# Optimization experiments

Measured on AMD Instinct MI355X. Metric: run time of the kernel, lower is better.

## Reference

```python
import jax, jax.numpy as jnp
import numpy as np

N_GRAPHS = 1250
NEG_SLOPE = 0.2

def gat_layer(x, src, dst, W, a_src, a_dst, b, concat):
    # x: [N, Fin]; W: [Fin, H*C]; a_src/a_dst: [H, C]; b: [H*C] or [C]
    N = x.shape[0]
    H, C = a_src.shape
    h = (x @ W).reshape(N, H, C)                      # [N,H,C]
    alpha_s = jnp.sum(h * a_src[None], axis=-1)       # [N,H]
    alpha_d = jnp.sum(h * a_dst[None], axis=-1)       # [N,H]
    e = jax.nn.leaky_relu(alpha_s[src] + alpha_d[dst], NEG_SLOPE)  # [E,H]
    # segment softmax over incoming edges of each target node
    m = jax.ops.segment_max(e, dst, num_segments=N)   # [N,H]
    m = jnp.where(jnp.isfinite(m), m, 0.0)
    ex = jnp.exp(e - m[dst])
    s = jax.ops.segment_sum(ex, dst, num_segments=N)  # [N,H]
    alpha = ex / (s[dst] + 1e-16)                     # [E,H]
    msg = h[src] * alpha[..., None]                   # [E,H,C]
    out = jax.ops.segment_sum(msg, dst, num_segments=N)  # [N,H,C]
    out = out.reshape(N, H * C) if concat else out.mean(axis=1)
    return out + b

def setup_inputs() -> dict:
    key = jax.random.key(0)
    ks = jax.random.split(key, 13)
    N, E = 50000, 100000
    x = jax.random.normal(ks[0], (N, 78), dtype=jnp.float32)
    edge_index = jax.random.randint(ks[1], (2, E), 0, N, dtype=jnp.int64)
    # sorted segment ids -> every graph non-empty (~40 nodes each)
    batch = jnp.sort(jax.random.randint(ks[2], (N,), 0, N_GRAPHS, dtype=jnp.int64))
    g = lambda k, shape, fan: jax.random.normal(k, shape, dtype=jnp.float32) / np.float32(np.sqrt(fan))
    return {
        'x': x, 'edge_index': edge_index, 'batch': batch,
        'W1': g(ks[3], (78, 780), 78), 'a_src1': g(ks[4], (10, 78), 78), 'a_dst1': g(ks[5], (10, 78), 78),
        'b1': jnp.zeros((780,), jnp.float32),
        'W2': g(ks[6], (780, 128), 780), 'a_src2': g(ks[7], (1, 128), 128), 'a_dst2': g(ks[8], (1, 128), 128),
        'b2': jnp.zeros((128,), jnp.float32),
        'fc_w': g(ks[9], (128, 128), 128), 'fc_b': jnp.zeros((128,), jnp.float32),
    }

def reference(x, edge_index, batch, W1, a_src1, a_dst1, b1, W2, a_src2, a_dst2, b2, fc_w, fc_b):
    N = x.shape[0]
    loop = jnp.arange(N, dtype=edge_index.dtype)
    src = jnp.concatenate([edge_index[0], loop])  # add self loops (PyG default)
    dst = jnp.concatenate([edge_index[1], loop])
    # dropout layers are identity in eval mode
    h = jax.nn.elu(gat_layer(x, src, dst, W1, a_src1, a_dst1, b1, concat=True))   # [N,780]
    h = jax.nn.relu(gat_layer(h, src, dst, W2, a_src2, a_dst2, b2, concat=True))  # [N,128]
    g = jax.ops.segment_max(h, batch, num_segments=N_GRAPHS)                      # [G,128]
    g = jnp.where(jnp.isfinite(g), g, 0.0)
    return jax.nn.relu(g @ fc_w + fc_b)
```

## Files before the change

kernel.cpp:

```cpp
#include <hip/hip_runtime.h>
#include <hip/hip_bf16.h>
#include <cstdint>

#define CAP 32
typedef __hip_bfloat16 bf16;
typedef __attribute__((ext_vector_type(8))) short short8;
typedef __attribute__((ext_vector_type(4))) float f32x4;

__device__ __forceinline__ float sb2f(short s) {
  unsigned int u = ((unsigned int)(unsigned short)s) << 16;
  return __uint_as_float(u);
}
__device__ __forceinline__ short f2sb(float f) {
  bf16 h = __float2bfloat16(f);
  return *reinterpret_cast<short*>(&h);
}

__global__ void k_detect(const int* __restrict__ ei, int* __restrict__ flag) {
  __shared__ int any;
  if (threadIdx.x == 0) any = 0;
  __syncthreads();
  int v = 0;
  for (int i = 1 + 2 * threadIdx.x; i < 2000; i += 512) v |= ei[i];
  if (v) atomicOr(&any, 1);
  __syncthreads();
  if (threadIdx.x == 0) flag[0] = (any == 0) ? 1 : 0;
}

__device__ __forceinline__ void edge_sd(const int* __restrict__ ei, int e, int f,
                                        int& src, int& dst) {
  if (e < 100000) {
    if (f) { src = ei[2 * e]; dst = ei[200000 + 2 * e]; }
    else   { src = ei[e];     dst = ei[100000 + e]; }
  } else { src = dst = e - 100000; }
  src = min(max(src, 0), 49999);
  dst = min(max(dst, 0), 49999);
}

__global__ void k_prep(const float* __restrict__ x, const float* __restrict__ W1,
                       const float* __restrict__ W2, const float* __restrict__ aw1,
                       const float* __restrict__ dw1, bf16* __restrict__ xb,
                       bf16* __restrict__ W1t, bf16* __restrict__ W2t,
                       bf16* __restrict__ Wat, float* __restrict__ zp, int zeroWords) {
  int i = blockIdx.x * 256 + threadIdx.x;
  if (i < zeroWords) zp[i] = 0.f;
  const int n_xb = 50000 * 96;
  const int n_w1 = 832 * 96;
  const int n_w2 = 128 * 832;
  const int n_wa = 32 * 96;
  if (i < n_xb) {
    int r = i / 96, k = i - r * 96;
    xb[i] = __float2bfloat16(k < 78 ? x[r * 78 + k] : 0.f);
  } else if (i < n_xb + n_w1) {
    int j = i - n_xb;
    int n = j / 96, k = j - n * 96;
    W1t[j] = __float2bfloat16((k < 78 && n < 780) ? W1[k * 780 + n] : 0.f);
  } else if (i < n_xb + n_w1 + n_w2) {
    int j = i - n_xb - n_w1;
    int c = j / 832, k = j - c * 832;
    W2t[j] = __float2bfloat16(k < 780 ? W2[k * 128 + c] : 0.f);
  } else if (i < n_xb + n_w1 + n_w2 + n_wa) {
    int j = i - n_xb - n_w1 - n_w2;
    int c = j / 96, k = j - c * 96;
    float s = 0.f;
    if (k < 78 && c < 20) {
      const float* w = (c < 10) ? aw1 : dw1;
      int h = (c < 10) ? c : c - 10;
      const float* wrow = W1 + k * 780 + h * 78;
      const float* arow = w + h * 78;
      for (int q = 0; q < 78; q++) s += wrow[q] * arow[q];
    }
    Wat[c * 96 + k] = __float2bfloat16(s);
  }
}

__global__ __launch_bounds__(256) void k_gemm1(const bf16* __restrict__ xb,
                                               const bf16* __restrict__ W1t,
                                               const bf16* __restrict__ Wat,
                                               bf16* __restrict__ H1,
                                               float* __restrict__ as1,
                                               float* __restrict__ ad1) {
  __shared__ __align__(16) short Als[64 * 104];
  __shared__ __align__(16) short Bls[64 * 104];
  __shared__ __align__(16) short Wls[32 * 104];
  __shared__ __align__(16) float Cls[64 * 68];
  const int t = threadIdx.x;
  const int w = t >> 6, l = t & 63, l15 = l & 15, q = l >> 4;
  const int rowBase = blockIdx.x * 64;
  for (int s = t; s < 768; s += 256) {
    int row = s / 12, kg = s - row * 12;
    short8 v = {};
    int gr = rowBase + row;
    if (gr < 50000) v = *(const short8*)((const short*)xb + (size_t)gr * 96 + kg * 8);
    *(short8*)&Als[row * 104 + kg * 8] = v;
  }
  for (int s = t; s < 384; s += 256) {
    int row = s / 12, kg = s - row * 12;
    *(short8*)&Wls[row * 104 + kg * 8] =
        *(const short8*)((const short*)Wat + (size_t)row * 96 + kg * 8);
  }
  short8 breg[3];
  int bn[3], bk[3];
#pragma unroll
  for (int i = 0; i < 3; i++) {
    int s = t + i * 256;
    bn[i] = s / 12; bk[i] = s - bn[i] * 12;
    breg[i] = *(const short8*)((const short*)W1t + (size_t)bn[i] * 96 + bk[i] * 8);
  }
  for (int cc = 0; cc < 13; cc++) {
    __syncthreads();
#pragma unroll
    for (int i = 0; i < 3; i++) *(short8*)&Bls[bn[i] * 104 + bk[i] * 8] = breg[i];
    if (cc < 12) {
#pragma unroll
      for (int i = 0; i < 3; i++)
        breg[i] = *(const short8*)((const short*)W1t +
                                   (size_t)((cc + 1) * 64 + bn[i]) * 96 + bk[i] * 8);
    }
    __syncthreads();
    f32x4 acc[4] = {};
#pragma unroll
    for (int ks = 0; ks < 3; ks++) {
      short8 a = *(const short8*)&Als[(w * 16 + l15) * 104 + ks * 32 + q * 8];
#pragma unroll
      for (int nt = 0; nt < 4; nt++) {
        short8 b = *(const short8*)&Bls[(nt * 16 + l15) * 104 + ks * 32 + q * 8];
        acc[nt] = __builtin_amdgcn_mfma_f32_16x16x32_bf16(a, b, acc[nt], 0, 0, 0);
      }
    }
    __syncthreads();
#pragma unroll
    for (int nt = 0; nt < 4; nt++)
#pragma unroll
      for (int r = 0; r < 4; r++)
        Cls[(w * 16 + q * 4 + r) * 68 + nt * 16 + l15] = acc[nt][r];
    __syncthreads();
    {
      int r = t >> 2, c0 = (t & 3) * 16;
      int gr = rowBase + r;
      if (gr < 50000) {
        short8 o0, o1;
#pragma unroll
        for (int c = 0; c < 8; c++) o0[c] = f2sb(Cls[r * 68 + c0 + c]);
#pragma unroll
        for (int c = 0; c < 8; c++) o1[c] = f2sb(Cls[r * 68 + c0 + 8 + c]);
        short* dst = (short*)H1 + (size_t)gr * 832 + cc * 64 + c0;
        *(short8*)dst = o0;
        *(short8*)(dst + 8) = o1;
      }
    }
  }
  f32x4 acc2[2] = {};
#pragma unroll
  for (int ks = 0; ks < 3; ks++) {
    short8 a = *(const short8*)&Als[(w * 16 + l15) * 104 + ks * 32 + q * 8];
#pragma unroll
    for (int nt = 0; nt < 2; nt++) {
      short8 b = *(const short8*)&Wls[(nt * 16 + l15) * 104 + ks * 32 + q * 8];
      acc2[nt] = __builtin_amdgcn_mfma_f32_16x16x32_bf16(a, b, acc2[nt], 0, 0, 0);
    }
  }
  const int gr0 = rowBase + w * 16 + q * 4;
#pragma unroll
  for (int nt = 0; nt < 2; nt++) {
    int c = nt * 16 + l15;
#pragma unroll
    for (int r = 0; r < 4; r++) {
      int gr = gr0 + r;
      if (gr < 50000) {
        if (c < 10)       as1[gr * 10 + c] = acc2[nt][r];
        else if (c < 20)  ad1[gr * 10 + (c - 10)] = acc2[nt][r];
      }
    }
  }
}

__global__ void k_scatter(const int* __restrict__ ei, const int* __restrict__ flag,
                          int* __restrict__ cnt, int* __restrict__ csr) {
  int e = blockIdx.x * 256 + threadIdx.x;
  if (e >= 150000) return;
  int f = flag[0], src, dst;
  edge_sd(ei, e, f, src, dst);
  int pos = atomicAdd(&cnt[dst], 1);
  if (pos < CAP) csr[dst * CAP + pos] = src;
}

__global__ __launch_bounds__(256) void k_agg1(const bf16* __restrict__ H1,
                                              const float* __restrict__ as1,
                                              const float* __restrict__ ad1,
                                              const int* __restrict__ csr,
                                              const int* __restrict__ cnt,
                                              const float* __restrict__ b1,
                                              bf16* __restrict__ HL2) {
  __shared__ float sexw[2][CAP * 10];
  __shared__ float sden[2][16];
  __shared__ float b1p[832];
  __shared__ int ssrc[2][CAP];
  __shared__ int scnt[2];
  const int t = threadIdx.x;
  const int sub = t >> 7, tt = t & 127;
  const int n = blockIdx.x * 2 + sub;
  if (t < 2) scnt[t] = min(cnt[blockIdx.x * 2 + t], CAP);
  if (t >= 32 && t < 64) { int z = t - 32; sden[z >> 4][z & 15] = 0.f; }
  for (int i = t; i < 832; i += 256) b1p[i] = (i < 780) ? b1[i] : 0.f;
  __syncthreads();
  const int cn = scnt[sub];
  if (tt < cn) ssrc[sub][tt] = csr[n * CAP + tt];
  __syncthreads();
  for (int wv = tt; wv < cn * 10; wv += 128) {
    int k = wv / 10, h = wv - k * 10;
    int src = ssrc[sub][k];
    float e = as1[src * 10 + h] + ad1[n * 10 + h];
    e = e >= 0.f ? e : 0.2f * e;
    float ex = __expf(e);
    sexw[sub][wv] = ex;
    atomicAdd(&sden[sub][h], ex);
  }
  __syncthreads();
  for (int wv = tt; wv < cn * 10; wv += 128) {
    int h = wv % 10;
    sexw[sub][wv] = sexw[sub][wv] / (sden[sub][h] + 1e-16f);
  }
  __syncthreads();
  if (tt < 104) {
    int hj[8];
#pragma unroll
    for (int c = 0; c < 8; c++) {
      int j = tt * 8 + c;
      int h = j / 78;
      hj[c] = h > 9 ? 9 : h;
    }
    float acc[8] = {};
    const float* sw = sexw[sub];
    const short* H1s = (const short*)H1;
    for (int k = 0; k < cn; k++) {
      int src = ssrc[sub][k];
      short8 hv = *(const short8*)(H1s + (size_t)src * 832 + tt * 8);
      const float* swk = sw + k * 10;
#pragma unroll
      for (int c = 0; c < 8; c++) acc[c] += swk[hj[c]] * sb2f(hv[c]);
    }
    short8 ov;
#pragma unroll
    for (int c = 0; c < 8; c++) {
      int j = tt * 8 + c;
      float v = acc[c] + b1p[j];
      v = v > 0.f ? v : __expf(v) - 1.f;
      ov[c] = f2sb(v);
    }
    *(short8*)((short*)HL2 + (size_t)n * 832 + tt * 8) = ov;
  }
}

__global__ __launch_bounds__(256) void k_gemm2(const bf16* __restrict__ A,
                                               const bf16* __restrict__ W2t,
                                               const float* __restrict__ AW2,
                                               const float* __restrict__ DW2,
                                               bf16* __restrict__ H2,
                                               float* __restrict__ as2,
                                               float* __restrict__ ad2) {
  __shared__ __align__(16) short Als[64 * 72];
  __shared__ __align__(16) short Bls[128 * 72];
  __shared__ float sAW[128], sDW[128];
  __shared__ float sS[4][64], sD[4][64];
  const int t = threadIdx.x;
  const int w = t >> 6, l = t & 63, l15 = l & 15, q = l >> 4;
  const int rowBase = blockIdx.x * 64;
  if (t < 128) sAW[t] = AW2[t];
  else         sDW[t - 128] = DW2[t - 128];
  const int ar = t >> 2, ak = t & 3;
  const int bc = t >> 1, bk2 = t & 1;
  short8 areg[2], breg[4];
  {
    int gr0 = rowBase + ar;
#pragma unroll
    for (int i = 0; i < 2; i++) {
      short8 v = {};
      int gr = gr0;
      if (gr < 50000)
        v = *(const short8*)((const short*)A + (size_t)gr * 832 + 0 + (ak * 2 + i) * 8);
      areg[i] = v;
    }
#pragma unroll
    for (int i = 0; i < 4; i++) {
      int s = t + i * 256;
      int col = s >> 3, kg = s & 7;
      breg[i] = *(const short8*)((const short*)W2t + (size_t)col * 832 + 0 + kg * 8);
    }
  }
  f32x4 acc[4][2] = {};
  for (int kb = 0; kb < 832; kb += 64) {
    __syncthreads();
#pragma unroll
    for (int i = 0; i < 2; i++)
      *(short8*)&Als[ar * 72 + (ak * 2 + i) * 8] = areg[i];
#pragma unroll
    for (int i = 0; i < 4; i++) {
      int s = t + i * 256;
      int col = s >> 3, kg = s & 7;
      *(short8*)&Bls[col * 72 + kg * 8] = breg[i];
    }
    if (kb < 768) {
      int kn = kb + 64;
      int gr = rowBase + ar;
#pragma unroll
      for (int i = 0; i < 2; i++) {
        short8 v = {};
        if (gr < 50000)
          v = *(const short8*)((const short*)A + (size_t)gr * 832 + kn + (ak * 2 + i) * 8);
        areg[i] = v;
      }
#pragma unroll
      for (int i = 0; i < 4; i++) {
        int s = t + i * 256;
        int col = s >> 3, kg = s & 7;
        breg[i] = *(const short8*)((const short*)W2t + (size_t)col * 832 + kn + kg * 8);
      }
    }
    __syncthreads();
#pragma unroll
    for (int ks = 0; ks < 2; ks++) {
      short8 a[4];
#pragma unroll
      for (int mt = 0; mt < 4; mt++)
        a[mt] = *(const short8*)&Als[(mt * 16 + l15) * 72 + ks * 32 + q * 8];
#pragma unroll
      for (int ntl = 0; ntl < 2; ntl++) {
        short8 b = *(const short8*)&Bls[((w * 2 + ntl) * 16 + l15) * 72 + ks * 32 + q * 8];
#pragma unroll
        for (int mt = 0; mt < 4; mt++)
          acc[mt][ntl] = __builtin_amdgcn_mfma_f32_16x16x32_bf16(a[mt], b, acc[mt][ntl], 0, 0, 0);
      }
    }
  }
  const int col0 = w * 32 + l15, col1 = col0 + 16;
  const float aw0 = sAW[col0], aw1 = sAW[col1];
  const float dw0 = sDW[col0], dw1 = sDW[col1];
  f32x4 sp[4], dp[4];
#pragma unroll
  for (int mt = 0; mt < 4; mt++) {
    sp[mt] = acc[mt][0] * aw0 + acc[mt][1] * aw1;
    dp[mt] = acc[mt][0] * dw0 + acc[mt][1] * dw1;
  }
#pragma unroll
  for (int m = 1; m < 16; m <<= 1) {
#pragma unroll
    for (int mt = 0; mt < 4; mt++)
#pragma unroll
      for (int r = 0; r < 4; r++) {
        sp[mt][r] += __shfl_xor(sp[mt][r], m, 64);
        dp[mt][r] += __shfl_xor(dp[mt][r], m, 64);
      }
  }
  if (l15 == 0) {
#pragma unroll
    for (int mt = 0; mt < 4; mt++)
#pragma unroll
      for (int r = 0; r < 4; r++) {
        sS[w][mt * 16 + q * 4 + r] = sp[mt][r];
        sD[w][mt * 16 + q * 4 + r] = dp[mt][r];
      }
  }
#pragma unroll
  for (int mt = 0; mt < 4; mt++) {
    int gr0 = rowBase + mt * 16 + q * 4;
#pragma unroll
    for (int ntl = 0; ntl < 2; ntl++) {
      int gc = w * 32 + ntl * 16 + l15;
#pragma unroll
      for (int r = 0; r < 4; r++) {
        int gr = gr0 + r;
        if (gr < 50000) H2[(size_t)gr * 128 + gc] = __float2bfloat16(acc[mt][ntl][r]);
      }
    }
  }
  __syncthreads();
  if (t < 64) {
    int gr = rowBase + t;
    if (gr < 50000) as2[gr] = sS[0][t] + sS[1][t] + sS[2][t] + sS[3][t];
  } else if (t < 128) {
    int r2 = t - 64;
    int gr = rowBase + r2;
    if (gr < 50000) ad2[gr] = sD[0][r2] + sD[1][r2] + sD[2][r2] + sD[3][r2];
  }
}

__global__ __launch_bounds__(256) void k_agg2(const bf16* __restrict__ H2,
                                              const float* __restrict__ as2,
                                              const float* __restrict__ ad2,
                                              const int* __restrict__ csr,
                                              const int* __restrict__ cnt,
                                              const float* __restrict__ b2,
                                              const int* __restrict__ batch,
                                              const int* __restrict__ flag,
                                              float* __restrict__ g) {
  __shared__ int ssrc[2][CAP];
  __shared__ float sexw[2][CAP];
  __shared__ float sden[2];
  __shared__ int scnt[2], sb[2];
  const int t = threadIdx.x;
  const int sub = t >> 7, tt = t & 127;
  const int n = blockIdx.x * 2 + sub;
  if (t < 2) {
    int nt2 = blockIdx.x * 2 + t;
    scnt[t] = min(cnt[nt2], CAP);
    sden[t] = 0.f;
    int b = flag[0] ? batch[2 * nt2] : batch[nt2];
    sb[t] = min(max(b, 0), 1249);
  }
  __syncthreads();
  const int cn = scnt[sub];
  if (tt < cn) {
    int src = csr[n * CAP + tt];
    ssrc[sub][tt] = src;
    float e = as2[src] + ad2[n];
    e = e >= 0.f ? e : 0.2f * e;
    float ex = __expf(e);
    sexw[sub][tt] = ex;
    atomicAdd(&sden[sub], ex);
  }
  __syncthreads();
  if (tt < cn) sexw[sub][tt] = sexw[sub][tt] / (sden[sub] + 1e-16f);
  __syncthreads();
  const short* H2s = (const short*)H2;
  float acc = 0.f;
  for (int k = 0; k < cn; k++)
    acc += sexw[sub][k] * sb2f(H2s[(size_t)ssrc[sub][k] * 128 + tt]);
  float v = acc + b2[tt];
  v = v > 0.f ? v : 0.f;
  atomicMax((int*)&g[sb[sub] * 128 + tt], __float_as_int(v));
}

__global__ __launch_bounds__(128) void k_fc(const float* __restrict__ g,
                                            const float* __restrict__ fw,
                                            const float* __restrict__ fb,
                                            float* __restrict__ out) {
  const int n = blockIdx.x, t = threadIdx.x;
  __shared__ float grow[128];
  grow[t] = g[n * 128 + t];
  __syncthreads();
  float acc = fb[t];
  for (int k = 0; k < 128; k++) acc += grow[k] * fw[k * 128 + t];
  out[n * 128 + t] = acc > 0.f ? acc : 0.f;
}

extern "C" void kernel_launch(void* const* d_in, const int* in_sizes, int n_in,
                              void* d_out, int out_size, void* d_ws, size_t ws_size,
                              hipStream_t stream) {
  const float* x     = (const float*)d_in[0];
  const int*   ei    = (const int*)d_in[1];
  const int*   batch = (const int*)d_in[2];
  const float* W1    = (const float*)d_in[3];
  const float* as1w  = (const float*)d_in[4];
  const float* ad1w  = (const float*)d_in[5];
  const float* b1    = (const float*)d_in[6];
  const float* W2    = (const float*)d_in[7];
  const float* as2w  = (const float*)d_in[8];
  const float* ad2w  = (const float*)d_in[9];
  const float* b2    = (const float*)d_in[10];
  const float* fcw   = (const float*)d_in[11];
  const float* fcb   = (const float*)d_in[12];
  float* out = (float*)d_out;

  char* p = (char*)d_ws;
  size_t off = 0;
  auto alloc = [&](size_t bytes) -> void* {
    void* r = p + off;
    off = (off + bytes + 15) & ~(size_t)15;
    return r;
  };
  int*   cnt = (int*)  alloc(50000 * 4);
  float* g   = (float*)alloc(160000 * 4);
  size_t zeroWords = off / 4;
  float* as1 = (float*)alloc(500000 * 4);
  float* ad1 = (float*)alloc(500000 * 4);
  float* as2 = (float*)alloc(50000 * 4);
  float* ad2 = (float*)alloc(50000 * 4);
  bf16*  W1t = (bf16*) alloc((size_t)832 * 96 * 2);
  bf16*  W2t = (bf16*) alloc((size_t)128 * 832 * 2);
  bf16*  Wat = (bf16*) alloc((size_t)32 * 96 * 2);
  bf16*  h1  = (bf16*) alloc((size_t)50000 * 832 * 2);
  bf16*  hl2 = (bf16*) alloc((size_t)50000 * 832 * 2);
  int*   csr = (int*)  alloc((size_t)50000 * CAP * 4);
  void*  uni = alloc((size_t)50000 * 128 * 2);
  bf16*  xb  = (bf16*)uni;
  bf16*  h2  = (bf16*)uni;
  int*   flag = (int*) alloc(16);
  (void)ws_size; (void)in_sizes; (void)n_in; (void)out_size;

  k_detect<<<1, 256, 0, stream>>>(ei, flag);
  int prepN = 50000 * 96 + 832 * 96 + 128 * 832 + 32 * 96;
  k_prep<<<(prepN + 255) / 256, 256, 0, stream>>>(
      x, W1, W2, as1w, ad1w, xb, W1t, W2t, Wat, (float*)d_ws, (int)zeroWords);

  k_gemm1<<<782, 256, 0, stream>>>(xb, W1t, Wat, h1, as1, ad1);
  k_scatter<<<(150000 + 255) / 256, 256, 0, stream>>>(ei, flag, cnt, csr);
  k_agg1<<<25000, 256, 0, stream>>>(h1, as1, ad1, csr, cnt, b1, hl2);
  k_gemm2<<<782, 256, 0, stream>>>(hl2, W2t, as2w, ad2w, h2, as2, ad2);
  k_agg2<<<25000, 256, 0, stream>>>(h2, as2, ad2, csr, cnt, b2, batch, flag, g);
  k_fc<<<1250, 128, 0, stream>>>(g, fcw, fcb, out);
}
```

Baseline: 294.8 us.

## Restructure GAT aggregation kernels: one node per block, prefetched gathers, deferred softmax normalization

The layer-1 bias add moves into the gemm1 epilogue. This is valid because the softmax weights sum to one per node, though the bias is now rounded into the bf16 H1 values. Both aggregation kernels now run one node per 128-thread block instead of two nodes per 256-thread block. They drop the separate normalization pass and divide by the denominator once at the end. The neighbour-row gathers are software-prefetched one or two steps ahead to hide memory latency. In agg1, attention logits come from vectorized float2 loads, and each thread's 8 features use at most two head weights instead of per-element head lookups.

```diff
diff --git a/kernel.cpp b/kernel.cpp
--- a/kernel.cpp
+++ b/kernel.cpp
@@ -77,6 +77,7 @@
 __global__ __launch_bounds__(256) void k_gemm1(const bf16* __restrict__ xb,
                                                const bf16* __restrict__ W1t,
                                                const bf16* __restrict__ Wat,
+                                               const float* __restrict__ b1,
                                                bf16* __restrict__ H1,
                                                float* __restrict__ as1,
                                                float* __restrict__ ad1) {
@@ -84,6 +85,7 @@
   __shared__ __align__(16) short Bls[64 * 104];
   __shared__ __align__(16) short Wls[32 * 104];
   __shared__ __align__(16) float Cls[64 * 68];
+  __shared__ float b1s[832];
   const int t = threadIdx.x;
   const int w = t >> 6, l = t & 63, l15 = l & 15, q = l >> 4;
   const int rowBase = blockIdx.x * 64;
@@ -99,6 +101,7 @@
     *(short8*)&Wls[row * 104 + kg * 8] =
         *(const short8*)((const short*)Wat + (size_t)row * 96 + kg * 8);
   }
+  for (int s = t; s < 832; s += 256) b1s[s] = (s < 780) ? b1[s] : 0.f;
   short8 breg[3];
   int bn[3], bk[3];
 #pragma unroll
@@ -141,9 +144,9 @@
       if (gr < 50000) {
         short8 o0, o1;
 #pragma unroll
-        for (int c = 0; c < 8; c++) o0[c] = f2sb(Cls[r * 68 + c0 + c]);
-#pragma unroll
-        for (int c = 0; c < 8; c++) o1[c] = f2sb(Cls[r * 68 + c0 + 8 + c]);
+        for (int c = 0; c < 8; c++) o0[c] = f2sb(Cls[r * 68 + c0 + c] + b1s[cc * 64 + c0 + c]);
+#pragma unroll
+        for (int c = 0; c < 8; c++) o1[c] = f2sb(Cls[r * 68 + c0 + 8 + c] + b1s[cc * 64 + c0 + 8 + c]);
         short* dst = (short*)H1 + (size_t)gr * 832 + cc * 64 + c0;
         *(short8*)dst = o0;
         *(short8*)(dst + 8) = o1;
@@ -185,70 +188,90 @@
   if (pos < CAP) csr[dst * CAP + pos] = src;
 }
 
-__global__ __launch_bounds__(256) void k_agg1(const bf16* __restrict__ H1,
+__global__ __launch_bounds__(128) void k_agg1(const bf16* __restrict__ H1,
                                               const float* __restrict__ as1,
                                               const float* __restrict__ ad1,
                                               const int* __restrict__ csr,
                                               const int* __restrict__ cnt,
-                                              const float* __restrict__ b1,
                                               bf16* __restrict__ HL2) {
-  __shared__ float sexw[2][CAP * 10];
-  __shared__ float sden[2][16];
-  __shared__ float b1p[832];
-  __shared__ int ssrc[2][CAP];
-  __shared__ int scnt[2];
+  __shared__ float sexw[CAP * 10];
+  __shared__ float sden[16];
+  __shared__ float sad[10];
+  __shared__ int ssrc[CAP];
+  __shared__ int scnt;
   const int t = threadIdx.x;
-  const int sub = t >> 7, tt = t & 127;
-  const int n = blockIdx.x * 2 + sub;
-  if (t < 2) scnt[t] = min(cnt[blockIdx.x * 2 + t], CAP);
-  if (t >= 32 && t < 64) { int z = t - 32; sden[z >> 4][z & 15] = 0.f; }
-  for (int i = t; i < 832; i += 256) b1p[i] = (i < 780) ? b1[i] : 0.f;
-  __syncthreads();
-  const int cn = scnt[sub];
-  if (tt < cn) ssrc[sub][tt] = csr[n * CAP + tt];
-  __syncthreads();
-  for (int wv = tt; wv < cn * 10; wv += 128) {
-    int k = wv / 10, h = wv - k * 10;
-    int src = ssrc[sub][k];
-    float e = as1[src * 10 + h] + ad1[n * 10 + h];
-    e = e >= 0.f ? e : 0.2f * e;
-    float ex = __expf(e);
-    sexw[sub][wv] = ex;
-    atomicAdd(&sden[sub][h], ex);
-  }
-  __syncthreads();
-  for (int wv = tt; wv < cn * 10; wv += 128) {
-    int h = wv % 10;
-    sexw[sub][wv] = sexw[sub][wv] / (sden[sub][h] + 1e-16f);
-  }
-  __syncthreads();
-  if (tt < 104) {
-    int hj[8];
+  const int n = blockIdx.x;
+  if (t == 0) scnt = min(cnt[n], CAP);
+  if (t >= 16 && t < 32) sden[t - 16] = 0.f;
+  if (t >= 32 && t < 42) sad[t - 32] = ad1[n * 10 + (t - 32)];
+  __syncthreads();
+  const int cn = scnt;
+  if (t < cn) {
+    int src = csr[n * CAP + t];
+    ssrc[t] = src;
+    const float2* ap = (const float2*)(as1 + src * 10);
+    float av[10];
+#pragma unroll
+    for (int i = 0; i < 5; i++) { float2 qq = ap[i]; av[2 * i] = qq.x; av[2 * i + 1] = qq.y; }
+#pragma unroll
+    for (int h = 0; h < 10; h++) {
+      float e = av[h] + sad[h];
+      e = e >= 0.f ? e : 0.2f * e;
+      float ex = __expf(e);
+      sexw[t * 10 + h] = ex;
+      atomicAdd(&sden[h], ex);
+    }
+  }
+  __syncthreads();
+  if (t < 104) {
+    const int j0 = t * 8;
+    const int h0u = j0 / 78;
+    const int hsplit = (h0u + 1) * 78 - j0;
+    const int h1u = (j0 + 7) / 78;
+    const int h0 = min(h0u, 9), h1 = min(h1u, 9);
+    const float* sw = sexw;
+    const short* base = (const short*)H1 + j0;
+    float acc[8] = {};
+    if (cn > 0) {
+      short8 v0 = *(const short8*)(base + (size_t)ssrc[0] * 832);
+      short8 v1 = v0;
+      if (cn > 1) v1 = *(const short8*)(base + (size_t)ssrc[1] * 832);
+      int k = 0;
+      for (; k + 2 < cn; k += 2) {
+        short8 p0 = *(const short8*)(base + (size_t)ssrc[k + 2] * 832);
+        short8 p1 = p0;
+        if (k + 3 < cn) p1 = *(const short8*)(base + (size_t)ssrc[k + 3] * 832);
+        {
+          float w0 = sw[k * 10 + h0], w1 = sw[k * 10 + h1];
+#pragma unroll
+          for (int c = 0; c < 8; c++) acc[c] += (c < hsplit ? w0 : w1) * sb2f(v0[c]);
+          float u0 = sw[(k + 1) * 10 + h0], u1 = sw[(k + 1) * 10 + h1];
+#pragma unroll
+          for (int c = 0; c < 8; c++) acc[c] += (c < hsplit ? u0 : u1) * sb2f(v1[c]);
+        }
+        v0 = p0; v1 = p1;
+      }
+      {
+        float w0 = sw[k * 10 + h0], w1 = sw[k * 10 + h1];
+#pragma unroll
+        for (int c = 0; c < 8; c++) acc[c] += (c < hsplit ? w0 : w1) * sb2f(v0[c]);
+      }
+      if (k + 1 < cn) {
+        float u0 = sw[(k + 1) * 10 + h0], u1 = sw[(k + 1) * 10 + h1];
+#pragma unroll
+        for (int c = 0; c < 8; c++) acc[c] += (c < hsplit ? u0 : u1) * sb2f(v1[c]);
+      }
+    }
+    const float r0 = 1.f / (sden[h0] + 1e-16f);
+    const float r1 = 1.f / (sden[h1] + 1e-16f);
+    short8 ov;
 #pragma unroll
     for (int c = 0; c < 8; c++) {
-      int j = tt * 8 + c;
-      int h = j / 78;
-      hj[c] = h > 9 ? 9 : h;
-    }
-    float acc[8] = {};
-    const float* sw = sexw[sub];
-    const short* H1s = (const short*)H1;
-    for (int k = 0; k < cn; k++) {
-      int src = ssrc[sub][k];
-      short8 hv = *(const short8*)(H1s + (size_t)src * 832 + tt * 8);
-      const float* swk = sw + k * 10;
-#pragma unroll
-      for (int c = 0; c < 8; c++) acc[c] += swk[hj[c]] * sb2f(hv[c]);
-    }
-    short8 ov;
-#pragma unroll
-    for (int c = 0; c < 8; c++) {
-      int j = tt * 8 + c;
-      float v = acc[c] + b1p[j];
+      float v = acc[c] * (c < hsplit ? r0 : r1);
       v = v > 0.f ? v : __expf(v) - 1.f;
       ov[c] = f2sb(v);
     }
-    *(short8*)((short*)HL2 + (size_t)n * 832 + tt * 8) = ov;
+    *(short8*)((short*)HL2 + (size_t)n * 832 + j0) = ov;
   }
 }
 
@@ -269,7 +292,6 @@
   if (t < 128) sAW[t] = AW2[t];
   else         sDW[t - 128] = DW2[t - 128];
   const int ar = t >> 2, ak = t & 3;
-  const int bc = t >> 1, bk2 = t & 1;
   short8 areg[2], breg[4];
   {
     int gr0 = rowBase + ar;
@@ -385,7 +407,7 @@
   }
 }
 
-__global__ __launch_bounds__(256) void k_agg2(const bf16* __restrict__ H2,
+__global__ __launch_bounds__(128) void k_agg2(const bf16* __restrict__ H2,
                                               const float* __restrict__ as2,
                                               const float* __restrict__ ad2,
                                               const int* __restrict__ csr,
@@ -394,41 +416,44 @@
                                               const int* __restrict__ batch,
                                               const int* __restrict__ flag,
                                               float* __restrict__ g) {
-  __shared__ int ssrc[2][CAP];
-  __shared__ float sexw[2][CAP];
-  __shared__ float sden[2];
-  __shared__ int scnt[2], sb[2];
+  __shared__ int ssrc[CAP];
+  __shared__ float sexw[CAP];
+  __shared__ float sden;
+  __shared__ int scnt, sbv;
   const int t = threadIdx.x;
-  const int sub = t >> 7, tt = t & 127;
-  const int n = blockIdx.x * 2 + sub;
-  if (t < 2) {
-    int nt2 = blockIdx.x * 2 + t;
-    scnt[t] = min(cnt[nt2], CAP);
-    sden[t] = 0.f;
-    int b = flag[0] ? batch[2 * nt2] : batch[nt2];
-    sb[t] = min(max(b, 0), 1249);
-  }
-  __syncthreads();
-  const int cn = scnt[sub];
-  if (tt < cn) {
-    int src = csr[n * CAP + tt];
-    ssrc[sub][tt] = src;
+  const int n = blockIdx.x;
+  if (t == 0) {
+    scnt = min(cnt[n], CAP);
+    sden = 0.f;
+    int b = flag[0] ? batch[2 * n] : batch[n];
+    sbv = min(max(b, 0), 1249);
+  }
+  __syncthreads();
+  const int cn = scnt;
+  if (t < cn) {
+    int src = csr[n * CAP + t];
+    ssrc[t] = src;
     float e = as2[src] + ad2[n];
     e = e >= 0.f ? e : 0.2f * e;
     float ex = __expf(e);
-    sexw[sub][tt] = ex;
-    atomicAdd(&sden[sub], ex);
-  }
-  __syncthreads();
-  if (tt < cn) sexw[sub][tt] = sexw[sub][tt] / (sden[sub] + 1e-16f);
+    sexw[t] = ex;
+    atomicAdd(&sden, ex);
+  }
   __syncthreads();
   const short* H2s = (const short*)H2;
   float acc = 0.f;
-  for (int k = 0; k < cn; k++)
-    acc += sexw[sub][k] * sb2f(H2s[(size_t)ssrc[sub][k] * 128 + tt]);
-  float v = acc + b2[tt];
+  if (cn > 0) {
+    short hv = H2s[(size_t)ssrc[0] * 128 + t];
+    for (int k = 0; k < cn; k++) {
+      short hn = hv;
+      if (k + 1 < cn) hn = H2s[(size_t)ssrc[k + 1] * 128 + t];
+      acc += sexw[k] * sb2f(hv);
+      hv = hn;
+    }
+  }
+  float v = acc / (sden + 1e-16f) + b2[t];
   v = v > 0.f ? v : 0.f;
-  atomicMax((int*)&g[sb[sub] * 128 + tt], __float_as_int(v));
+  atomicMax((int*)&g[sbv * 128 + t], __float_as_int(v));
 }
 
 __global__ __launch_bounds__(128) void k_fc(const float* __restrict__ g,
@@ -493,10 +518,10 @@
   k_prep<<<(prepN + 255) / 256, 256, 0, stream>>>(
       x, W1, W2, as1w, ad1w, xb, W1t, W2t, Wat, (float*)d_ws, (int)zeroWords);
 
-  k_gemm1<<<782, 256, 0, stream>>>(xb, W1t, Wat, h1, as1, ad1);
+  k_gemm1<<<782, 256, 0, stream>>>(xb, W1t, Wat, b1, h1, as1, ad1);
   k_scatter<<<(150000 + 255) / 256, 256, 0, stream>>>(ei, flag, cnt, csr);
-  k_agg1<<<25000, 256, 0, stream>>>(h1, as1, ad1, csr, cnt, b1, hl2);
+  k_agg1<<<50000, 128, 0, stream>>>(h1, as1, ad1, csr, cnt, hl2);
   k_gemm2<<<782, 256, 0, stream>>>(hl2, W2t, as2w, ad2w, h2, as2, ad2);
-  k_agg2<<<25000, 256, 0, stream>>>(h2, as2, ad2, csr, cnt, b2, batch, flag, g);
+  k_agg2<<<50000, 128, 0, stream>>>(h2, as2, ad2, csr, cnt, b2, batch, flag, g);
   k_fc<<<1250, 128, 0, stream>>>(g, fcw, fcb, out);
 }
```

Measured after the change: 310.0 us. 5.1% more time.
